# Performance work log

Hardware: AMD Instinct MI355X
Metric: run time of the kernel (lower is better)

The kernel has to match this reference:

```python
import jax, jax.numpy as jnp
import numpy as np

B, K, D, LS, NL = 32, 64, 256, 128, 2


def _xavier(key, shape):
    # torch xavier_uniform for Linear weight [out, in]
    fan_out, fan_in = shape[-2], shape[-1]
    lim = float(np.sqrt(6.0 / (fan_in + fan_out)))
    return jax.random.uniform(key, shape, jnp.float32, -lim, lim)


def setup_inputs():
    key = jax.random.key(0)
    ks = jax.random.split(key, 32)
    inp = {
        "X": jax.random.normal(ks[0], (B, K, D), jnp.float32),
        # per-layer stacked params [NL, ...]
        "k_w": _xavier(ks[1], (NL, D, D)),
        "q_w": _xavier(ks[2], (NL, D, D)),
        "rv_w1": _xavier(ks[3], (NL, D, 2 * D)),
        "rv_b1": jnp.zeros((NL, D), jnp.float32),
        "rv_w2": _xavier(ks[4], (NL, D, D)),
        "rv_b2": jnp.zeros((NL, D), jnp.float32),
        "ln_g": jnp.ones((NL, D), jnp.float32),
        "ln_b": jnp.zeros((NL, D), jnp.float32),
        "mlp_w1": _xavier(ks[5], (NL, D, D)),
        "mlp_b1": jnp.zeros((NL, D), jnp.float32),
        "mlp_w2": _xavier(ks[6], (NL, D, D)),
        "mlp_b2": jnp.zeros((NL, D), jnp.float32),
        "proj_w": _xavier(ks[7], (LS, D)),
        "proj_b": jnp.zeros((LS,), jnp.float32),
        "mu_w": _xavier(ks[8], (LS, LS)),
        "mu_b": jnp.zeros((LS,), jnp.float32),
        "sp_w": _xavier(ks[9], (LS, LS)),
        "sp_b": jnp.zeros((LS,), jnp.float32),
    }
    return inp


def _gelu(x):
    return jax.nn.gelu(x, approximate=False)


def _layernorm(x, g, b, eps=1e-5):
    m = jnp.mean(x, axis=-1, keepdims=True)
    v = jnp.mean((x - m) ** 2, axis=-1, keepdims=True)
    return (x - m) / jnp.sqrt(v + eps) * g + b


def _block(x, kw, qw, rw1, rb1, rw2, rb2, lg, lb, mw1, mb1, mw2, mb2):
    scale = D ** (-0.5)
    x_orig = x
    # pairwise difference r[b,i,j,:] = x[b,i]-x[b,j]
    r = x[:, :, None, :] - x[:, None, :, :]                      # [B,K,K,D]
    xi = jnp.broadcast_to(x[:, :, None, :], (B, K, K, D))
    cat = jnp.concatenate([xi, r], axis=-1)                      # [B,K,K,2D]
    v = _gelu(jnp.einsum('bijc,dc->bijd', cat, rw1) + rb1)
    v = jnp.einsum('bijd,ed->bije', v, rw2) + rb2                # [B,K,K,D]
    k = jnp.einsum('bid,ed->bie', x, kw)
    q = jnp.einsum('bid,ed->bie', x, qw) * scale
    attn = jax.nn.softmax(jnp.einsum('bid,bjd->bij', q, k), axis=2)
    agg = jnp.einsum('bij,bijd->bid', attn, v)
    h = _layernorm(x_orig + agg, lg, lb)
    h = jnp.einsum('bid,ed->bie', _gelu(jnp.einsum('bid,ed->bie', h, mw1) + mb1), mw2) + mb2
    return x_orig + h


def reference(X, k_w, q_w, rv_w1, rv_b1, rv_w2, rv_b2, ln_g, ln_b,
              mlp_w1, mlp_b1, mlp_w2, mlp_b2, proj_w, proj_b,
              mu_w, mu_b, sp_w, sp_b):
    x = X
    for i in range(NL):
        x = _block(x, k_w[i], q_w[i], rv_w1[i], rv_b1[i], rv_w2[i], rv_b2[i],
                   ln_g[i], ln_b[i], mlp_w1[i], mlp_b1[i], mlp_w2[i], mlp_b2[i])
    s = jnp.sum(x, axis=1)                                        # [B,D]
    h = _gelu(s @ proj_w.T + proj_b)                              # [B,LS]
    mu = h @ mu_w.T + mu_b
    scale = jax.nn.softplus(h @ sp_w.T + sp_b)
    return (mu, scale)
```

## Files before the change

### kernel.cpp

```cpp
#include <hip/hip_runtime.h>
#include <hip/hip_bf16.h>


using bf16 = __hip_bfloat16;
typedef short bf16x8 __attribute__((ext_vector_type(8)));
typedef float f32x4 __attribute__((ext_vector_type(4)));

__device__ __forceinline__ float bfu(unsigned short u) { return __uint_as_float(((unsigned)u) << 16); }

__device__ __forceinline__ unsigned short bfr(float v) {
  unsigned u = __float_as_uint(v);
  u += 0x7FFFu + ((u >> 16) & 1u);
  return (unsigned short)(u >> 16);
}

__device__ __forceinline__ float gelu_e(float x) {
  return 0.5f * x * (1.0f + erff(x * 0.7071067811865475f));
}

__device__ __forceinline__ float load_f(const void* p, int i, int fl) {
  if (fl) return bfu(((const unsigned short*)p)[i]);
  return ((const float*)p)[i];
}

__device__ __forceinline__ int block_detect(const void* X) {
  __shared__ int bad_s;
  if (threadIdx.x == 0) bad_s = 0;
  __syncthreads();
  if (threadIdx.x < 256) {
    const float v = bfu(((const unsigned short*)X)[threadIdx.x]);
    if (!(fabsf(v) < 1e6f)) atomicOr(&bad_s, 1);
  }
  __syncthreads();
  return bad_s ? 0 : 1;
}

__device__ __forceinline__ void stage_split4(unsigned short (&aF)[2][4096], int row, int d0, float4 v) {
  ushort4 h, lo;
  h.x = bfr(v.x); h.y = bfr(v.y); h.z = bfr(v.z); h.w = bfr(v.w);
  lo.x = bfr(v.x - bfu(h.x)); lo.y = bfr(v.y - bfu(h.y));
  lo.z = bfr(v.z - bfu(h.z)); lo.w = bfr(v.w - bfu(h.w));
  const int kt = d0 >> 5, lane = row | (((d0 >> 3) & 3) << 4), j = d0 & 7;
  *(ushort4*)&aF[0][kt*512 + lane*8 + j] = h;
  *(ushort4*)&aF[1][kt*512 + lane*8 + j] = lo;
}

__device__ void prep_phase(
    int blk, int t, int fl, char* psm,
    const void* kw, const void* qw, const void* rw1, const void* rw2,
    const void* mw1, const void* mw2, const void* pw, const void* muw, const void* spw,
    const void* rb1, const void* rb2, const void* lng, const void* lnb,
    const void* mb1, const void* mb2, const void* pb, const void* mub, const void* spb,
    unsigned short* wfb, unsigned short* w3b, float* wh, float* bc)
{
  if (blk < 16) {
    unsigned short* ls = (unsigned short*)psm;
    unsigned* lsu = (unsigned*)psm;
    const int l = blk >> 3, kt = blk & 7;
    #pragma unroll
    for (int pass = 0; pass < 2; ++pass) {
      if (pass == 0) {
        if (fl) {
          #pragma unroll
          for (int s = 0; s < 2; ++s) {
            const unsigned* sp = (const unsigned*)((s == 0) ? kw : qw);
            for (int i = t; i < 4096; i += 512) {
              const int e = i >> 4, d2 = i & 15;
              lsu[s*4096 + i] = sp[(l*256 + e)*128 + kt*16 + d2];
            }
          }
        } else {
          #pragma unroll
          for (int s = 0; s < 2; ++s) {
            const float* sp = (const float*)((s == 0) ? kw : qw);
            for (int i = t; i < 4096; i += 512) {
              const int e = i >> 4, d2 = i & 15;
              const float f0 = sp[(l*256 + e)*256 + kt*32 + d2*2];
              const float f1 = sp[(l*256 + e)*256 + kt*32 + d2*2 + 1];
              lsu[s*4096 + i] = (unsigned)bfr(f0) | ((unsigned)bfr(f1) << 16);
            }
          }
        }
      } else {
        if (fl) {
          const unsigned* sp = (const unsigned*)rw1;
          #pragma unroll
          for (int s = 0; s < 2; ++s)
            for (int i = t; i < 4096; i += 512) {
              const int e = i >> 4, d2 = i & 15;
              lsu[s*4096 + i] = sp[(l*256 + e)*256 + s*128 + kt*16 + d2];
            }
        } else {
          const float* sp = (const float*)rw1;
          #pragma unroll
          for (int s = 0; s < 2; ++s)
            for (int i = t; i < 4096; i += 512) {
              const int e = i >> 4, d2 = i & 15;
              const float f0 = sp[(l*256 + e)*512 + s*256 + kt*32 + d2*2];
              const float f1 = sp[(l*256 + e)*512 + s*256 + kt*32 + d2*2 + 1];
              lsu[s*4096 + i] = (unsigned)bfr(f0) | ((unsigned)bfr(f1) << 16);
            }
        }
      }
      __syncthreads();
      unsigned* outp = (unsigned*)wfb + (l*8 + kt)*16384 + pass*8192;
      for (int f2 = t; f2 < 8192; f2 += 512) {
        const int j2 = f2 & 3, lane = (f2 >> 2) & 63, ntl = f2 >> 8;
        const int seg = ntl >> 4;
        const int e = (ntl & 15)*16 + (lane & 15);
        const int dl = ((lane >> 4) & 3)*8 + j2*2;
        unsigned short r0 = ls[seg*8192 + e*32 + dl];
        unsigned short r1 = ls[seg*8192 + e*32 + dl + 1];
        if (pass == 1 && seg == 0) {
          const unsigned short w0 = ls[8192 + e*32 + dl];
          const unsigned short w1 = ls[8192 + e*32 + dl + 1];
          r0 = bfr(bfu(r0) + bfu(w0)); r1 = bfr(bfu(r1) + bfu(w1));
        }
        outp[f2] = (unsigned)r0 | ((unsigned)r1 << 16);
      }
      __syncthreads();
    }
    return;
  }
  int b2 = blk - 16;
  if (b2 < 48) {
    unsigned short* ls = (unsigned short*)psm;
    unsigned* lsu = (unsigned*)psm;
    const int l3 = b2 >> 3, kt = b2 & 7;
    const int l = l3 / 3, gm = l3 % 3;
    const void* src = (gm == 0) ? rw2 : (gm == 1) ? mw1 : mw2;
    if (fl) {
      const unsigned* sp = (const unsigned*)src;
      for (int i = t; i < 4096; i += 512) {
        const int e = i >> 4, d2 = i & 15;
        lsu[i] = sp[(l*256 + e)*128 + kt*16 + d2];
      }
    } else {
      const float* sp = (const float*)src;
      for (int i = t; i < 4096; i += 512) {
        const int e = i >> 4, d2 = i & 15;
        const float f0 = sp[(l*256 + e)*256 + kt*32 + d2*2];
        const float f1 = sp[(l*256 + e)*256 + kt*32 + d2*2 + 1];
        lsu[i] = (unsigned)bfr(f0) | ((unsigned)bfr(f1) << 16);
      }
    }
    __syncthreads();
    unsigned* outp = (unsigned*)w3b + (l3*8 + kt)*4096;
    for (int f2 = t; f2 < 4096; f2 += 512) {
      const int j2 = f2 & 3, lane = (f2 >> 2) & 63, nt = f2 >> 8;
      const int e = nt*16 + (lane & 15);
      const int dl = ((lane >> 4) & 3)*8 + j2*2;
      outp[f2] = (unsigned)ls[e*32 + dl] | ((unsigned)ls[e*32 + dl + 1] << 16);
    }
    return;
  }
  b2 -= 48;
  if (b2 < 24) {
    float* lsf = (float*)psm;
    if (b2 < 8) {
      const int l0 = b2*16;
      if (fl) {
        const unsigned* sp = (const unsigned*)pw;
        for (int i = t; i < 2048; i += 512) {
          const int ll = i >> 7, d2 = i & 127;
          const unsigned u = sp[(l0 + ll)*128 + d2];
          lsf[ll*256 + d2*2]     = __uint_as_float(u << 16);
          lsf[ll*256 + d2*2 + 1] = __uint_as_float(u & 0xffff0000u);
        }
      } else {
        const float* sp = (const float*)pw;
        for (int i = t; i < 4096; i += 512) {
          const int ll = i >> 8, d = i & 255;
          lsf[ll*256 + d] = sp[(l0 + ll)*256 + d];
        }
      }
      __syncthreads();
      for (int i = t; i < 4096; i += 512) {
        const int d = i >> 4, ll = i & 15;
        wh[d*128 + l0 + ll] = lsf[ll*256 + d];
      }
    } else {
      const int grp2 = b2 - 8;
      const int isSp = grp2 >> 3;
      const int l0 = (grp2 & 7)*16;
      const void* src = isSp ? spw : muw;
      const int off = isSp ? 49152 : 32768;
      if (fl) {
        const unsigned* sp = (const unsigned*)src;
        for (int i = t; i < 1024; i += 512) {
          const int ll = i >> 6, c2 = i & 63;
          const unsigned u = sp[(l0 + ll)*64 + c2];
          lsf[ll*128 + c2*2]     = __uint_as_float(u << 16);
          lsf[ll*128 + c2*2 + 1] = __uint_as_float(u & 0xffff0000u);
        }
      } else {
        const float* sp = (const float*)src;
        for (int i = t; i < 2048; i += 512) {
          const int ll = i >> 7, c = i & 127;
          lsf[ll*128 + c] = sp[(l0 + ll)*128 + c];
        }
      }
      __syncthreads();
      for (int i = t; i < 2048; i += 512) {
        const int c = i >> 4, ll = i & 15;
        wh[off + c*128 + l0 + ll] = lsf[ll*128 + c];
      }
    }
    return;
  }
  if (b2 == 24) {
    for (int i = t; i < 3456; i += 512) {
      const void* src; int off;
      if (i < 512)       { src = rb1; off = i; }
      else if (i < 1024) { src = rb2; off = i - 512; }
      else if (i < 1536) { src = lng; off = i - 1024; }
      else if (i < 2048) { src = lnb; off = i - 1536; }
      else if (i < 2560) { src = mb1; off = i - 2048; }
      else if (i < 3072) { src = mb2; off = i - 2560; }
      else if (i < 3200) { src = pb;  off = i - 3072; }
      else if (i < 3328) { src = mub; off = i - 3200; }
      else               { src = spb; off = i - 3328; }
      bc[i] = load_f(src, off, fl);
    }
  }
}

__device__ __forceinline__ bf16x8 raw_bfrag(int seg, int e, int d0, int fl,
    const void* kw, const void* qw, const void* rw1)
{
  if (fl) {
    if (seg == 0) return *(const bf16x8*)((const unsigned short*)kw + e*256 + d0);
    if (seg == 1) return *(const bf16x8*)((const unsigned short*)qw + e*256 + d0);
    const unsigned short* r1 = (const unsigned short*)rw1 + e*512;
    const bf16x8 wb = *(const bf16x8*)(r1 + 256 + d0);
    if (seg == 3) return wb;
    const bf16x8 wa = *(const bf16x8*)(r1 + d0);
    bf16x8 r;
    #pragma unroll
    for (int i = 0; i < 8; ++i)
      r[i] = (short)bfr(bfu((unsigned short)wa[i]) + bfu((unsigned short)wb[i]));
    return r;
  } else {
    float vs[8];
    if (seg <= 1) {
      const float* sp = (const float*)((seg == 0) ? kw : qw) + e*256 + d0;
      #pragma unroll
      for (int i = 0; i < 8; ++i) vs[i] = sp[i];
    } else {
      const float* r1 = (const float*)rw1 + e*512;
      #pragma unroll
      for (int i = 0; i < 8; ++i) vs[i] = r1[256 + d0 + i];
      if (seg == 2) {
        #pragma unroll
        for (int i = 0; i < 8; ++i) vs[i] += r1[d0 + i];
      }
    }
    bf16x8 r;
    #pragma unroll
    for (int i = 0; i < 8; ++i) r[i] = (short)bfr(vs[i]);
    return r;
  }
}

template<bool SPLIT>
__device__ void k1_raw(const unsigned short (&aF)[2][4096], int seg, int ntg0,
    const void* kw, const void* qw, const void* rw1, const void* rb1, int fl,
    float* __restrict__ kq, float* __restrict__ Pf, unsigned* __restrict__ Qpk,
    int row0, int t)
{
  const int w = t >> 6, l64 = t & 63;
  const int col = l64 & 15, quad = l64 >> 4;
  f32x4 acc[2];
  acc[0] = (f32x4){0.f, 0.f, 0.f, 0.f};
  acc[1] = (f32x4){0.f, 0.f, 0.f, 0.f};
  for (int kt = 0; kt < 8; ++kt) {
    const bf16x8 ah = *(const bf16x8*)&aF[0][kt*512 + l64*8];
    bf16x8 al;
    if (SPLIT) al = *(const bf16x8*)&aF[1][kt*512 + l64*8];
    const int d0 = kt*32 + quad*8;
    #pragma unroll
    for (int i = 0; i < 2; ++i) {
      const int ntg = ntg0 + w*2 + i;
      const int e = (ntg & 15)*16 + col;
      const bf16x8 b = raw_bfrag(seg, e, d0, fl, kw, qw, rw1);
      acc[i] = __builtin_amdgcn_mfma_f32_16x16x32_bf16(ah, b, acc[i], 0, 0, 0);
      if (SPLIT) acc[i] = __builtin_amdgcn_mfma_f32_16x16x32_bf16(al, b, acc[i], 0, 0, 0);
    }
  }
  #pragma unroll
  for (int i = 0; i < 2; ++i) {
    const int ntg = ntg0 + w*2 + i;
    if (seg < 2) {
      const int n = ntg*16 + col;
      #pragma unroll
      for (int r = 0; r < 4; ++r)
        kq[(size_t)(row0 + quad*4 + r)*512 + n] = acc[i][r];
    } else if (seg == 2) {
      const int c = (ntg & 15)*16 + col;
      const float bias = load_f(rb1, c, fl);
      #pragma unroll
      for (int r = 0; r < 4; ++r)
        Pf[(size_t)(row0 + quad*4 + r)*256 + c] = acc[i][r] + bias;
    } else {
      #pragma unroll
      for (int r = 0; r < 4; ++r) {
        const float v = acc[i][r];
        const float pv = __shfl_xor(v, 1, 64);
        if (!(col & 1)) {
          const unsigned uu = (unsigned)bfr(v) | ((unsigned)bfr(pv) << 16);
          Qpk[(size_t)(row0 + quad*4 + r)*128 + (ntg & 15)*8 + (col >> 1)] = uu;
        }
      }
    }
  }
}

__global__ __launch_bounds__(512) void fusedA(
    const void* __restrict__ X, const void* __restrict__ kw, const void* __restrict__ qw,
    const void* __restrict__ rw1, const void* __restrict__ rw2, const void* __restrict__ mw1,
    const void* __restrict__ mw2, const void* __restrict__ pw, const void* __restrict__ muw,
    const void* __restrict__ spw,
    const void* __restrict__ rb1, const void* __restrict__ rb2, const void* __restrict__ lng,
    const void* __restrict__ lnb, const void* __restrict__ mb1, const void* __restrict__ mb2,
    const void* __restrict__ pb, const void* __restrict__ mub, const void* __restrict__ spb,
    unsigned short* __restrict__ wfb, unsigned short* __restrict__ w3b,
    float* __restrict__ wh, float* __restrict__ bc,
    float* __restrict__ kq, float* __restrict__ Pf, unsigned* __restrict__ Qpk)
{
  __shared__ __align__(16) char smem[32768];
  const int fl = block_detect(X);
  const int t = threadIdx.x;
  const int blk = blockIdx.x;
  if (blk < 89) {
    prep_phase(blk, t, fl, smem, kw, qw, rw1, rw2, mw1, mw2, pw, muw, spw,
               rb1, rb2, lng, lnb, mb1, mb2, pb, mub, spb, wfb, w3b, wh, bc);
    return;
  }
  auto& aF = *(unsigned short(*)[2][4096])smem;
  const int rb = blk - 89;
  const int mb = rb >> 2, seg = rb & 3;
  const int row0 = mb * 16, ntg0 = seg * 16;
  if (fl) {
    const int row = t >> 5, d0 = (t & 31) * 8;
    const uint4 u = *(const uint4*)((const unsigned*)X + (size_t)(row0 + row)*128 + (t & 31)*4);
    const int kt = d0 >> 5, lane = row | (((d0 >> 3) & 3) << 4);
    *(uint4*)&aF[0][kt*512 + lane*8] = u;
  } else {
    for (int i = t; i < 1024; i += 512) {
      const int row = i >> 6, d0 = (i & 63) * 4;
      stage_split4(aF, row, d0, *(const float4*)((const float*)X + (size_t)(row0 + row)*256 + d0));
    }
  }
  __syncthreads();
  if (fl) k1_raw<false>(aF, seg, ntg0, kw, qw, rw1, rb1, fl, kq, Pf, Qpk, row0, t);
  else    k1_raw<true >(aF, seg, ntg0, kw, qw, rw1, rb1, fl, kq, Pf, Qpk, row0, t);
}

template<bool SPLIT, int NTG>
__device__ __forceinline__ void k1_body(
    const unsigned short (&aF)[2][4096],
    const unsigned short* __restrict__ wfb, const float* __restrict__ bc,
    float* __restrict__ kq, float* __restrict__ Pf, unsigned* __restrict__ Qpk,
    int l, int row0, int ntg0, int t)
{
  const int w = t >> 6, l64 = t & 63;
  const int col = l64 & 15, quad = l64 >> 4;
  f32x4 acc[NTG];
  #pragma unroll
  for (int i = 0; i < NTG; ++i) acc[i] = (f32x4){0.f, 0.f, 0.f, 0.f};
  for (int kt = 0; kt < 8; ++kt) {
    const bf16x8 ah = *(const bf16x8*)&aF[0][kt*512 + l64*8];
    bf16x8 al;
    if (SPLIT) al = *(const bf16x8*)&aF[1][kt*512 + l64*8];
    #pragma unroll
    for (int i = 0; i < NTG; ++i) {
      const int ntg = ntg0 + w*NTG + i;
      const bf16x8 b = *(const bf16x8*)&wfb[((l*8 + kt)*64 + ntg)*512 + l64*8];
      acc[i] = __builtin_amdgcn_mfma_f32_16x16x32_bf16(ah, b, acc[i], 0, 0, 0);
      if (SPLIT) acc[i] = __builtin_amdgcn_mfma_f32_16x16x32_bf16(al, b, acc[i], 0, 0, 0);
    }
  }
  #pragma unroll
  for (int i = 0; i < NTG; ++i) {
    const int ntg = ntg0 + w*NTG + i;
    if (ntg < 32) {
      const int n = ntg*16 + col;
      #pragma unroll
      for (int r = 0; r < 4; ++r)
        kq[(size_t)(row0 + quad*4 + r)*512 + n] = acc[i][r];
    } else if (ntg < 48) {
      const int c = (ntg - 32)*16 + col;
      const float bias = bc[l*256 + c];
      #pragma unroll
      for (int r = 0; r < 4; ++r)
        Pf[(size_t)(row0 + quad*4 + r)*256 + c] = acc[i][r] + bias;
    } else {
      #pragma unroll
      for (int r = 0; r < 4; ++r) {
        const float v = acc[i][r];
        const float pv = __shfl_xor(v, 1, 64);
        if (!(col & 1)) {
          const unsigned uu = (unsigned)bfr(v) | ((unsigned)bfr(pv) << 16);
          Qpk[(size_t)(row0 + quad*4 + r)*128 + (ntg - 48)*8 + (col >> 1)] = uu;
        }
      }
    }
  }
}

__global__ __launch_bounds__(256) void k23_attn(
    const float* __restrict__ kq, const float* __restrict__ Pf,
    const unsigned* __restrict__ Qpk, float* __restrict__ g,
    float* __restrict__ ssacc, unsigned* __restrict__ cnt, int doZero)
{
  __shared__ float qs[2][256];
  __shared__ float scp[2][64];
  __shared__ float als[2][64];
  const int t = threadIdx.x;
  const int b = (int)blockIdx.x >> 5, ip = (int)blockIdx.x & 31;
  const int base = b << 6, i0 = ip * 2;
  if (doZero && ip == 0) {
    ssacc[b*256 + t] = 0.f;
    if (t == 0) cnt[b] = 0u;
  }
  for (int i = t; i < 512; i += 256)
    qs[i >> 8][i & 255] = kq[(size_t)(base + i0 + (i >> 8))*512 + 256 + (i & 255)];
  __syncthreads();
  {
    const int w = t >> 6, lane = t & 63;
    const int jl = lane & 15, part = lane >> 4;
    const int j = w*16 + jl;
    const float* krow = kq + (size_t)(base + j)*512 + part*64;
    const float* q0p = &qs[0][part*64];
    const float* q1p = &qs[1][part*64];
    float s0 = 0.f, s1 = 0.f;
    for (int dd = 0; dd < 64; dd += 4) {
      const float4 kv = *(const float4*)&krow[dd];
      const float4 q0 = *(const float4*)&q0p[dd];
      const float4 q1 = *(const float4*)&q1p[dd];
      s0 = fmaf(kv.x, q0.x, s0); s0 = fmaf(kv.y, q0.y, s0);
      s0 = fmaf(kv.z, q0.z, s0); s0 = fmaf(kv.w, q0.w, s0);
      s1 = fmaf(kv.x, q1.x, s1); s1 = fmaf(kv.y, q1.y, s1);
      s1 = fmaf(kv.z, q1.z, s1); s1 = fmaf(kv.w, q1.w, s1);
    }
    s0 += __shfl_xor(s0, 16, 64); s0 += __shfl_xor(s0, 32, 64);
    s1 += __shfl_xor(s1, 16, 64); s1 += __shfl_xor(s1, 32, 64);
    if (part == 0) { scp[0][j] = s0 * 0.0625f; scp[1][j] = s1 * 0.0625f; }
  }
  __syncthreads();
  if (t < 128) {
    const int row = t >> 6, j = t & 63;
    float s = scp[row][j];
    float m = s;
    #pragma unroll
    for (int off = 32; off; off >>= 1) m = fmaxf(m, __shfl_xor(m, off, 64));
    const float e = __expf(s - m);
    float ss = e;
    #pragma unroll
    for (int off = 32; off; off >>= 1) ss += __shfl_xor(ss, off, 64);
    als[row][j] = e / ss;
  }
  __syncthreads();
  const int rg = t >> 7, cp = t & 127;
  const int r = base + i0 + rg;
  const float2 P = *(const float2*)&Pf[(size_t)r*256 + cp*2];
  const float A0 = -1.702f * P.x, A1 = -1.702f * P.y;
  const float* ap = &als[rg][0];
  const unsigned* qp = Qpk + (size_t)base*128 + cp;
  float acc0 = 0.f, acc1 = 0.f;
  #pragma unroll 8
  for (int j = 0; j < 64; ++j) {
    const unsigned u = qp[j*128];
    const float wgt = ap[j];
    const float q0 = __uint_as_float(u << 16);
    const float q1 = __uint_as_float(u & 0xffff0000u);
    const float s0 = __builtin_amdgcn_rcpf(1.f + __expf(fmaf(1.702f, q0, A0)));
    const float s1 = __builtin_amdgcn_rcpf(1.f + __expf(fmaf(1.702f, q1, A1)));
    acc0 = fmaf(wgt * (P.x - q0), s0, acc0);
    acc1 = fmaf(wgt * (P.y - q1), s1, acc1);
  }
  *(float2*)&g[(size_t)r*256 + cp*2] = make_float2(acc0, acc1);
}

__device__ __forceinline__ void k4_gemm8(
    f32x4 acc[2], const unsigned short (&aF)[2][4096],
    const unsigned short* __restrict__ wg, int w, int l64)
{
  acc[0] = (f32x4){0.f, 0.f, 0.f, 0.f};
  acc[1] = (f32x4){0.f, 0.f, 0.f, 0.f};
  for (int kt = 0; kt < 8; ++kt) {
    const bf16x8 ah = *(const bf16x8*)&aF[0][kt*512 + l64*8];
    const bf16x8 al = *(const bf16x8*)&aF[1][kt*512 + l64*8];
    #pragma unroll
    for (int nt = 0; nt < 2; ++nt) {
      const bf16x8 b = *(const bf16x8*)&wg[((kt*16 + (w*2 + nt))*64 + l64)*8];
      acc[nt] = __builtin_amdgcn_mfma_f32_16x16x32_bf16(ah, b, acc[nt], 0, 0, 0);
      acc[nt] = __builtin_amdgcn_mfma_f32_16x16x32_bf16(al, b, acc[nt], 0, 0, 0);
    }
  }
}

template<bool ADAPT, bool TAIL, int NR>
__device__ __forceinline__ void k4_core(
    const float* __restrict__ g, const void* __restrict__ xin, int fl,
    float* __restrict__ xout, const unsigned short* __restrict__ wg,
    const float* __restrict__ bc, int l, int row0, int t, bool writeX,
    unsigned short (&aF)[2][4096], float* bufB, float (&mv)[16][2])
{
  const int w = t >> 6, l64 = t & 63;
  const int col = l64 & 15, quad = l64 >> 4;
  const float* rb2c = bc + 512  + l*256;
  const float* lngc = bc + 1024 + l*256;
  const float* lnbc = bc + 1536 + l*256;
  const float* mb1c = bc + 2048 + l*256;
  const float* mb2c = bc + 2560 + l*256;

  for (int i = t; i < NR*64; i += 512) {
    const int row = i >> 6, d0 = (i & 63) * 4;
    stage_split4(aF, row, d0, *(const float4*)&g[(size_t)(row0 + row)*256 + d0]);
  }
  if (ADAPT && fl) {
    for (int c = t; c < NR*128; c += 512) {
      const int row = c >> 7, dp = c & 127;
      const unsigned u = ((const unsigned*)xin)[(size_t)(row0 + row)*128 + dp];
      bufB[row*260 + dp*2]     = __uint_as_float(u << 16);
      bufB[row*260 + dp*2 + 1] = __uint_as_float(u & 0xffff0000u);
    }
  } else {
    for (int c = t; c < NR*64; c += 512) {
      const int row = c >> 6, d0 = (c & 63) * 4;
      *(float4*)&bufB[row*260 + d0] = *(const float4*)((const float*)xin + (size_t)(row0 + row)*256 + d0);
    }
  }
  __syncthreads();
  float xtr[2][4];
  #pragma unroll
  for (int nt = 0; nt < 2; ++nt) {
    const int cn = (w*2 + nt)*16 + col;
    #pragma unroll
    for (int r = 0; r < 4; ++r) xtr[nt][r] = bufB[(quad*4 + r)*260 + cn];
  }
  __syncthreads();

  f32x4 acc[2];
  k4_gemm8(acc, aF, wg, w, l64);
  #pragma unroll
  for (int nt = 0; nt < 2; ++nt) {
    const int cn = (w*2 + nt)*16 + col;
    #pragma unroll
    for (int r = 0; r < 4; ++r)
      bufB[(quad*4 + r)*260 + cn] = acc[nt][r] + rb2c[cn] + xtr[nt][r];
  }
  __syncthreads();
  {
    const int row = t >> 5, part = t & 31;
    if (row < NR) {
      float s = 0.f, s2 = 0.f;
      #pragma unroll
      for (int kk = 0; kk < 8; ++kk) {
        const float v = bufB[row*260 + part + kk*32];
        s += v; s2 = fmaf(v, v, s2);
      }
      #pragma unroll
      for (int off = 16; off; off >>= 1) {
        s  += __shfl_xor(s, off, 32);
        s2 += __shfl_xor(s2, off, 32);
      }
      if (part == 0) {
        const float mu = s * (1.f/256.f);
        mv[row][0] = mu;
        mv[row][1] = rsqrtf(fmaf(-mu, mu, s2 * (1.f/256.f)) + 1e-5f);
      }
    }
  }
  __syncthreads();
  for (int i = t; i < NR*64; i += 512) {
    const int row = i >> 6, d0 = (i & 63) * 4;
    float4 v = *(const float4*)&bufB[row*260 + d0];
    const float m = mv[row][0], iv = mv[row][1];
    v.x = (v.x - m)*iv*lngc[d0]   + lnbc[d0];
    v.y = (v.y - m)*iv*lngc[d0+1] + lnbc[d0+1];
    v.z = (v.z - m)*iv*lngc[d0+2] + lnbc[d0+2];
    v.w = (v.w - m)*iv*lngc[d0+3] + lnbc[d0+3];
    stage_split4(aF, row, d0, v);
  }
  __syncthreads();
  k4_gemm8(acc, aF, wg + 65536, w, l64);
  #pragma unroll
  for (int nt = 0; nt < 2; ++nt) {
    const int cn = (w*2 + nt)*16 + col;
    #pragma unroll
    for (int r = 0; r < 4; ++r)
      if (quad*4 + r < NR)
        bufB[(quad*4 + r)*260 + cn] = gelu_e(acc[nt][r] + mb1c[cn]);
  }
  __syncthreads();
  for (int i = t; i < NR*64; i += 512) {
    const int row = i >> 6, d0 = (i & 63) * 4;
    stage_split4(aF, row, d0, *(const float4*)&bufB[row*260 + d0]);
  }
  __syncthreads();
  k4_gemm8(acc, aF, wg + 2*65536, w, l64);
  if (TAIL) {
    #pragma unroll
    for (int nt = 0; nt < 2; ++nt) {
      const int cn = (w*2 + nt)*16 + col;
      #pragma unroll
      for (int r = 0; r < 4; ++r)
        bufB[(quad*4 + r)*260 + cn] = acc[nt][r] + mb2c[cn] + xtr[nt][r];
    }
    __syncthreads();
    for (int i = t; i < NR*64; i += 512) {
      const int row = i >> 6, d0 = (i & 63) * 4;
      const float4 v = *(const float4*)&bufB[row*260 + d0];
      if (writeX) *(float4*)&xout[(size_t)(row0 + row)*256 + d0] = v;
      stage_split4(aF, row, d0, v);
    }
    __syncthreads();
  } else {
    #pragma unroll
    for (int nt = 0; nt < 2; ++nt) {
      const int cn = (w*2 + nt)*16 + col;
      #pragma unroll
      for (int r = 0; r < 4; ++r)
        if (quad*4 + r < NR)
          xout[(size_t)(row0 + quad*4 + r)*256 + cn] = acc[nt][r] + mb2c[cn] + xtr[nt][r];
    }
  }
}

__global__ __launch_bounds__(512) void k41_mix_kq(
    const float* __restrict__ g, const unsigned short* __restrict__ w3b,
    const unsigned short* __restrict__ wfb, const float* __restrict__ bc,
    const void* __restrict__ X, float* __restrict__ x,
    float* __restrict__ kq, float* __restrict__ Pf, unsigned* __restrict__ Qpk)
{
  const int fl = block_detect(X);
  __shared__ __align__(16) unsigned short aF[2][4096];
  __shared__ float bufB[16*260];
  __shared__ float mv[16][2];
  const int t = threadIdx.x;
  const int rb = (int)blockIdx.x >> 1, parity = (int)blockIdx.x & 1;
  const int row0 = rb * 16;
  k4_core<true, true, 16>(g, X, fl, x, w3b, bc, 0, row0, t, parity == 0, aF, bufB, mv);
  k1_body<true, 4>(aF, wfb, bc, kq, Pf, Qpk, 1, row0, parity*32, t);
}

__global__ __launch_bounds__(512) void k4_fin_head(
    const float* __restrict__ g, const unsigned short* __restrict__ w3b,
    const float* __restrict__ bc, float* __restrict__ x,
    const float* __restrict__ wh, float* __restrict__ ssacc,
    unsigned* __restrict__ cnt, const void* __restrict__ X,
    void* __restrict__ out)
{
  const int fl = block_detect(X);
  __shared__ __align__(16) unsigned short aF[2][4096];
  __shared__ float bufB[16*260];
  __shared__ float mv[16][2];
  __shared__ int lastf;
  const int t = threadIdx.x;
  const int row0 = (int)blockIdx.x * 8;
  const int b = (int)blockIdx.x >> 3;
  k4_core<false, true, 8>(g, x, 0, x, w3b + 3*65536, bc, 1, row0, t, false, aF, bufB, mv);
  if (t < 256) {
    float cs = 0.f;
    #pragma unroll
    for (int r = 0; r < 8; ++r) cs += bufB[r*260 + t];
    atomicAdd(&ssacc[b*256 + t], cs);
  }
  __syncthreads();
  if (t == 0) lastf = (atomicAdd(&cnt[b], 1u) == 7u);
  __syncthreads();
  if (!lastf) return;
  float* ss = bufB;
  float* hh = bufB + 256;
  if (t < 256)
    ss[t] = __hip_atomic_load(&ssacc[b*256 + t], __ATOMIC_RELAXED, __HIP_MEMORY_SCOPE_AGENT);
  __syncthreads();
  if (t < 128) {
    float acc = bc[3072 + t];
    const float* projT = wh;
    for (int d = 0; d < 256; ++d) acc = fmaf(ss[d], projT[d*128 + t], acc);
    hh[t] = gelu_e(acc);
  }
  __syncthreads();
  if (t < 256) {
    float v; int oidx;
    if (t < 128) {
      float acc = bc[3200 + t];
      const float* muT = wh + 32768;
      for (int c = 0; c < 128; ++c) acc = fmaf(hh[c], muT[c*128 + t], acc);
      v = acc; oidx = b*128 + t;
    } else {
      const int u = t - 128;
      float acc = bc[3328 + u];
      const float* spT = wh + 49152;
      for (int c = 0; c < 128; ++c) acc = fmaf(hh[c], spT[c*128 + u], acc);
      v = (acc > 20.f) ? acc : log1pf(__expf(acc));
      oidx = 4096 + b*128 + u;
    }
    if (fl) ((bf16*)out)[oidx] = __float2bfloat16(v);
    else    ((float*)out)[oidx] = v;
  }
}

extern "C" void kernel_launch(void* const* d_in, const int* in_sizes, int n_in,
                              void* d_out, int out_size, void* d_ws, size_t ws_size,
                              hipStream_t stream)
{
  (void)in_sizes; (void)n_in; (void)out_size; (void)ws_size;
  float* ws    = (float*)d_ws;
  float* x     = ws + 16;
  float* kq    = x + 524288;
  float* Pf    = kq + 1048576;
  unsigned* Qpk = (unsigned*)(Pf + 524288);
  float* g     = (float*)(Qpk + 262144);
  unsigned short* wfb = (unsigned short*)(g + 524288);
  unsigned short* w3b = wfb + 524288;
  float* wh    = (float*)(w3b + 393216);
  float* bc    = wh + 65536;
  float* ssacc = bc + 4096;
  unsigned* cnt = (unsigned*)(ssacc + 8192);

  fusedA<<<dim3(601), dim3(512), 0, stream>>>(
      d_in[0], d_in[1], d_in[2], d_in[3], d_in[5], d_in[9], d_in[11],
      d_in[13], d_in[15], d_in[17],
      d_in[4], d_in[6], d_in[7], d_in[8], d_in[10], d_in[12],
      d_in[14], d_in[16], d_in[18],
      wfb, w3b, wh, bc, kq, Pf, Qpk);
  k23_attn<<<dim3(1024), dim3(256), 0, stream>>>(kq, Pf, Qpk, g, ssacc, cnt, 0);
  k41_mix_kq<<<dim3(256), dim3(512), 0, stream>>>(g, w3b, wfb, bc, d_in[0], x, kq, Pf, Qpk);
  k23_attn<<<dim3(1024), dim3(256), 0, stream>>>(kq, Pf, Qpk, g, ssacc, cnt, 1);
  k4_fin_head<<<dim3(256), dim3(512), 0, stream>>>(g, w3b, bc, x, wh, ssacc, cnt, d_in[0], (void*)d_out);
}
```

Before: 212.2 us.

## Fuse attention with the following MLP stage via last-arriver counters, cutting launches

Merges the attention kernel with the per-row-tile mix/MLP kernel. Each group of four attention blocks covering a 16-row tile increments a counter, and the last block to arrive runs the LayerNorm/MLP and next-layer projections for that tile. kq/Pf/Qpk are double-buffered so the fused kernel can write the next layer's inputs without racing readers. Counter and accumulator zeroing moves into the prep phase, and layer-0 weight repacking blocks are dropped. This removes two launches and their inter-kernel gaps. In exchange it serializes the tail work onto fewer blocks and relies on threadfence/atomic ordering.

```diff
diff --git a/kernel.cpp b/kernel.cpp
--- a/kernel.cpp
+++ b/kernel.cpp
@@ -51,12 +51,13 @@
     const void* mw1, const void* mw2, const void* pw, const void* muw, const void* spw,
     const void* rb1, const void* rb2, const void* lng, const void* lnb,
     const void* mb1, const void* mb2, const void* pb, const void* mub, const void* spb,
-    unsigned short* wfb, unsigned short* w3b, float* wh, float* bc)
-{
-  if (blk < 16) {
+    unsigned short* wfb, unsigned short* w3b, float* wh, float* bc,
+    unsigned* cnts, float* ssacc)
+{
+  if (blk < 8) {
     unsigned short* ls = (unsigned short*)psm;
     unsigned* lsu = (unsigned*)psm;
-    const int l = blk >> 3, kt = blk & 7;
+    const int l = 1, kt = blk;
     #pragma unroll
     for (int pass = 0; pass < 2; ++pass) {
       if (pass == 0) {
@@ -103,7 +104,7 @@
         }
       }
       __syncthreads();
-      unsigned* outp = (unsigned*)wfb + (l*8 + kt)*16384 + pass*8192;
+      unsigned* outp = (unsigned*)wfb + (8 + kt)*16384 + pass*8192;
       for (int f2 = t; f2 < 8192; f2 += 512) {
         const int j2 = f2 & 3, lane = (f2 >> 2) & 63, ntl = f2 >> 8;
         const int seg = ntl >> 4;
@@ -122,7 +123,7 @@
     }
     return;
   }
-  int b2 = blk - 16;
+  int b2 = blk - 8;
   if (b2 < 48) {
     unsigned short* ls = (unsigned short*)psm;
     unsigned* lsu = (unsigned*)psm;
@@ -222,6 +223,8 @@
       else               { src = spb; off = i - 3328; }
       bc[i] = load_f(src, off, fl);
     }
+    for (int i = t; i < 288; i += 512) cnts[i] = 0u;
+    for (int i = t; i < 8192; i += 512) ssacc[i] = 0.f;
   }
 }
 
@@ -325,19 +328,21 @@
     const void* __restrict__ pb, const void* __restrict__ mub, const void* __restrict__ spb,
     unsigned short* __restrict__ wfb, unsigned short* __restrict__ w3b,
     float* __restrict__ wh, float* __restrict__ bc,
-    float* __restrict__ kq, float* __restrict__ Pf, unsigned* __restrict__ Qpk)
+    unsigned* __restrict__ cnts, float* __restrict__ ssacc,
+    float* __restrict__ kqA, float* __restrict__ PfA, unsigned* __restrict__ QpkA)
 {
   __shared__ __align__(16) char smem[32768];
   const int fl = block_detect(X);
   const int t = threadIdx.x;
   const int blk = blockIdx.x;
-  if (blk < 89) {
+  if (blk < 81) {
     prep_phase(blk, t, fl, smem, kw, qw, rw1, rw2, mw1, mw2, pw, muw, spw,
-               rb1, rb2, lng, lnb, mb1, mb2, pb, mub, spb, wfb, w3b, wh, bc);
+               rb1, rb2, lng, lnb, mb1, mb2, pb, mub, spb, wfb, w3b, wh, bc,
+               cnts, ssacc);
     return;
   }
   auto& aF = *(unsigned short(*)[2][4096])smem;
-  const int rb = blk - 89;
+  const int rb = blk - 81;
   const int mb = rb >> 2, seg = rb & 3;
   const int row0 = mb * 16, ntg0 = seg * 16;
   if (fl) {
@@ -352,8 +357,8 @@
     }
   }
   __syncthreads();
-  if (fl) k1_raw<false>(aF, seg, ntg0, kw, qw, rw1, rb1, fl, kq, Pf, Qpk, row0, t);
-  else    k1_raw<true >(aF, seg, ntg0, kw, qw, rw1, rb1, fl, kq, Pf, Qpk, row0, t);
+  if (fl) k1_raw<false>(aF, seg, ntg0, kw, qw, rw1, rb1, fl, kqA, PfA, QpkA, row0, t);
+  else    k1_raw<true >(aF, seg, ntg0, kw, qw, rw1, rb1, fl, kqA, PfA, QpkA, row0, t);
 }
 
 template<bool SPLIT, int NTG>
@@ -408,80 +413,6 @@
   }
 }
 
-__global__ __launch_bounds__(256) void k23_attn(
-    const float* __restrict__ kq, const float* __restrict__ Pf,
-    const unsigned* __restrict__ Qpk, float* __restrict__ g,
-    float* __restrict__ ssacc, unsigned* __restrict__ cnt, int doZero)
-{
-  __shared__ float qs[2][256];
-  __shared__ float scp[2][64];
-  __shared__ float als[2][64];
-  const int t = threadIdx.x;
-  const int b = (int)blockIdx.x >> 5, ip = (int)blockIdx.x & 31;
-  const int base = b << 6, i0 = ip * 2;
-  if (doZero && ip == 0) {
-    ssacc[b*256 + t] = 0.f;
-    if (t == 0) cnt[b] = 0u;
-  }
-  for (int i = t; i < 512; i += 256)
-    qs[i >> 8][i & 255] = kq[(size_t)(base + i0 + (i >> 8))*512 + 256 + (i & 255)];
-  __syncthreads();
-  {
-    const int w = t >> 6, lane = t & 63;
-    const int jl = lane & 15, part = lane >> 4;
-    const int j = w*16 + jl;
-    const float* krow = kq + (size_t)(base + j)*512 + part*64;
-    const float* q0p = &qs[0][part*64];
-    const float* q1p = &qs[1][part*64];
-    float s0 = 0.f, s1 = 0.f;
-    for (int dd = 0; dd < 64; dd += 4) {
-      const float4 kv = *(const float4*)&krow[dd];
-      const float4 q0 = *(const float4*)&q0p[dd];
-      const float4 q1 = *(const float4*)&q1p[dd];
-      s0 = fmaf(kv.x, q0.x, s0); s0 = fmaf(kv.y, q0.y, s0);
-      s0 = fmaf(kv.z, q0.z, s0); s0 = fmaf(kv.w, q0.w, s0);
-      s1 = fmaf(kv.x, q1.x, s1); s1 = fmaf(kv.y, q1.y, s1);
-      s1 = fmaf(kv.z, q1.z, s1); s1 = fmaf(kv.w, q1.w, s1);
-    }
-    s0 += __shfl_xor(s0, 16, 64); s0 += __shfl_xor(s0, 32, 64);
-    s1 += __shfl_xor(s1, 16, 64); s1 += __shfl_xor(s1, 32, 64);
-    if (part == 0) { scp[0][j] = s0 * 0.0625f; scp[1][j] = s1 * 0.0625f; }
-  }
-  __syncthreads();
-  if (t < 128) {
-    const int row = t >> 6, j = t & 63;
-    float s = scp[row][j];
-    float m = s;
-    #pragma unroll
-    for (int off = 32; off; off >>= 1) m = fmaxf(m, __shfl_xor(m, off, 64));
-    const float e = __expf(s - m);
-    float ss = e;
-    #pragma unroll
-    for (int off = 32; off; off >>= 1) ss += __shfl_xor(ss, off, 64);
-    als[row][j] = e / ss;
-  }
-  __syncthreads();
-  const int rg = t >> 7, cp = t & 127;
-  const int r = base + i0 + rg;
-  const float2 P = *(const float2*)&Pf[(size_t)r*256 + cp*2];
-  const float A0 = -1.702f * P.x, A1 = -1.702f * P.y;
-  const float* ap = &als[rg][0];
-  const unsigned* qp = Qpk + (size_t)base*128 + cp;
-  float acc0 = 0.f, acc1 = 0.f;
-  #pragma unroll 8
-  for (int j = 0; j < 64; ++j) {
-    const unsigned u = qp[j*128];
-    const float wgt = ap[j];
-    const float q0 = __uint_as_float(u << 16);
-    const float q1 = __uint_as_float(u & 0xffff0000u);
-    const float s0 = __builtin_amdgcn_rcpf(1.f + __expf(fmaf(1.702f, q0, A0)));
-    const float s1 = __builtin_amdgcn_rcpf(1.f + __expf(fmaf(1.702f, q1, A1)));
-    acc0 = fmaf(wgt * (P.x - q0), s0, acc0);
-    acc1 = fmaf(wgt * (P.y - q1), s1, acc1);
-  }
-  *(float2*)&g[(size_t)r*256 + cp*2] = make_float2(acc0, acc1);
-}
-
 __device__ __forceinline__ void k4_gemm8(
     f32x4 acc[2], const unsigned short (&aF)[2][4096],
     const unsigned short* __restrict__ wg, int w, int l64)
@@ -500,7 +431,7 @@
   }
 }
 
-template<bool ADAPT, bool TAIL, int NR>
+template<bool ADAPT>
 __device__ __forceinline__ void k4_core(
     const float* __restrict__ g, const void* __restrict__ xin, int fl,
     float* __restrict__ xout, const unsigned short* __restrict__ wg,
@@ -515,19 +446,19 @@
   const float* mb1c = bc + 2048 + l*256;
   const float* mb2c = bc + 2560 + l*256;
 
-  for (int i = t; i < NR*64; i += 512) {
+  for (int i = t; i < 1024; i += 512) {
     const int row = i >> 6, d0 = (i & 63) * 4;
     stage_split4(aF, row, d0, *(const float4*)&g[(size_t)(row0 + row)*256 + d0]);
   }
   if (ADAPT && fl) {
-    for (int c = t; c < NR*128; c += 512) {
+    for (int c = t; c < 2048; c += 512) {
       const int row = c >> 7, dp = c & 127;
       const unsigned u = ((const unsigned*)xin)[(size_t)(row0 + row)*128 + dp];
       bufB[row*260 + dp*2]     = __uint_as_float(u << 16);
       bufB[row*260 + dp*2 + 1] = __uint_as_float(u & 0xffff0000u);
     }
   } else {
-    for (int c = t; c < NR*64; c += 512) {
+    for (int c = t; c < 1024; c += 512) {
       const int row = c >> 6, d0 = (c & 63) * 4;
       *(float4*)&bufB[row*260 + d0] = *(const float4*)((const float*)xin + (size_t)(row0 + row)*256 + d0);
     }
@@ -554,27 +485,25 @@
   __syncthreads();
   {
     const int row = t >> 5, part = t & 31;
-    if (row < NR) {
-      float s = 0.f, s2 = 0.f;
-      #pragma unroll
-      for (int kk = 0; kk < 8; ++kk) {
-        const float v = bufB[row*260 + part + kk*32];
-        s += v; s2 = fmaf(v, v, s2);
-      }
-      #pragma unroll
-      for (int off = 16; off; off >>= 1) {
-        s  += __shfl_xor(s, off, 32);
-        s2 += __shfl_xor(s2, off, 32);
-      }
-      if (part == 0) {
-        const float mu = s * (1.f/256.f);
-        mv[row][0] = mu;
-        mv[row][1] = rsqrtf(fmaf(-mu, mu, s2 * (1.f/256.f)) + 1e-5f);
-      }
-    }
-  }
-  __syncthreads();
-  for (int i = t; i < NR*64; i += 512) {
+    float s = 0.f, s2 = 0.f;
+    #pragma unroll
+    for (int kk = 0; kk < 8; ++kk) {
+      const float v = bufB[row*260 + part + kk*32];
+      s += v; s2 = fmaf(v, v, s2);
+    }
+    #pragma unroll
+    for (int off = 16; off; off >>= 1) {
+      s  += __shfl_xor(s, off, 32);
+      s2 += __shfl_xor(s2, off, 32);
+    }
+    if (part == 0) {
+      const float mu = s * (1.f/256.f);
+      mv[row][0] = mu;
+      mv[row][1] = rsqrtf(fmaf(-mu, mu, s2 * (1.f/256.f)) + 1e-5f);
+    }
+  }
+  __syncthreads();
+  for (int i = t; i < 1024; i += 512) {
     const int row = i >> 6, d0 = (i & 63) * 4;
     float4 v = *(const float4*)&bufB[row*260 + d0];
     const float m = mv[row][0], iv = mv[row][1];
@@ -591,87 +520,138 @@
     const int cn = (w*2 + nt)*16 + col;
     #pragma unroll
     for (int r = 0; r < 4; ++r)
-      if (quad*4 + r < NR)
-        bufB[(quad*4 + r)*260 + cn] = gelu_e(acc[nt][r] + mb1c[cn]);
-  }
-  __syncthreads();
-  for (int i = t; i < NR*64; i += 512) {
+      bufB[(quad*4 + r)*260 + cn] = gelu_e(acc[nt][r] + mb1c[cn]);
+  }
+  __syncthreads();
+  for (int i = t; i < 1024; i += 512) {
     const int row = i >> 6, d0 = (i & 63) * 4;
     stage_split4(aF, row, d0, *(const float4*)&bufB[row*260 + d0]);
   }
   __syncthreads();
   k4_gemm8(acc, aF, wg + 2*65536, w, l64);
-  if (TAIL) {
-    #pragma unroll
-    for (int nt = 0; nt < 2; ++nt) {
-      const int cn = (w*2 + nt)*16 + col;
-      #pragma unroll
-      for (int r = 0; r < 4; ++r)
-        bufB[(quad*4 + r)*260 + cn] = acc[nt][r] + mb2c[cn] + xtr[nt][r];
-    }
-    __syncthreads();
-    for (int i = t; i < NR*64; i += 512) {
-      const int row = i >> 6, d0 = (i & 63) * 4;
-      const float4 v = *(const float4*)&bufB[row*260 + d0];
-      if (writeX) *(float4*)&xout[(size_t)(row0 + row)*256 + d0] = v;
-      stage_split4(aF, row, d0, v);
-    }
-    __syncthreads();
-  } else {
-    #pragma unroll
-    for (int nt = 0; nt < 2; ++nt) {
-      const int cn = (w*2 + nt)*16 + col;
-      #pragma unroll
-      for (int r = 0; r < 4; ++r)
-        if (quad*4 + r < NR)
-          xout[(size_t)(row0 + quad*4 + r)*256 + cn] = acc[nt][r] + mb2c[cn] + xtr[nt][r];
-    }
-  }
-}
-
-__global__ __launch_bounds__(512) void k41_mix_kq(
-    const float* __restrict__ g, const unsigned short* __restrict__ w3b,
-    const unsigned short* __restrict__ wfb, const float* __restrict__ bc,
+  #pragma unroll
+  for (int nt = 0; nt < 2; ++nt) {
+    const int cn = (w*2 + nt)*16 + col;
+    #pragma unroll
+    for (int r = 0; r < 4; ++r)
+      bufB[(quad*4 + r)*260 + cn] = acc[nt][r] + mb2c[cn] + xtr[nt][r];
+  }
+  __syncthreads();
+  for (int i = t; i < 1024; i += 512) {
+    const int row = i >> 6, d0 = (i & 63) * 4;
+    const float4 v = *(const float4*)&bufB[row*260 + d0];
+    if (writeX) *(float4*)&xout[(size_t)(row0 + row)*256 + d0] = v;
+    stage_split4(aF, row, d0, v);
+  }
+  __syncthreads();
+}
+
+__global__ __launch_bounds__(512) void k23m(
+    const float* __restrict__ kq, const float* __restrict__ Pf,
+    const unsigned* __restrict__ Qpk, float* __restrict__ g,
     const void* __restrict__ X, float* __restrict__ x,
-    float* __restrict__ kq, float* __restrict__ Pf, unsigned* __restrict__ Qpk)
-{
+    const unsigned short* __restrict__ w3b, const unsigned short* __restrict__ wfb,
+    const float* __restrict__ bc, const float* __restrict__ wh,
+    float* __restrict__ kqO, float* __restrict__ PfO, unsigned* __restrict__ QpkO,
+    float* __restrict__ ssacc, unsigned* __restrict__ cnts,
+    void* __restrict__ out, int mode)
+{
+  __shared__ __align__(16) char smem[33280];
+  __shared__ float mv[16][2];
+  __shared__ int winf;
   const int fl = block_detect(X);
-  __shared__ __align__(16) unsigned short aF[2][4096];
-  __shared__ float bufB[16*260];
-  __shared__ float mv[16][2];
   const int t = threadIdx.x;
-  const int rb = (int)blockIdx.x >> 1, parity = (int)blockIdx.x & 1;
-  const int row0 = rb * 16;
-  k4_core<true, true, 16>(g, X, fl, x, w3b, bc, 0, row0, t, parity == 0, aF, bufB, mv);
-  k1_body<true, 4>(aF, wfb, bc, kq, Pf, Qpk, 1, row0, parity*32, t);
-}
-
-__global__ __launch_bounds__(512) void k4_fin_head(
-    const float* __restrict__ g, const unsigned short* __restrict__ w3b,
-    const float* __restrict__ bc, float* __restrict__ x,
-    const float* __restrict__ wh, float* __restrict__ ssacc,
-    unsigned* __restrict__ cnt, const void* __restrict__ X,
-    void* __restrict__ out)
-{
-  const int fl = block_detect(X);
-  __shared__ __align__(16) unsigned short aF[2][4096];
-  __shared__ float bufB[16*260];
-  __shared__ float mv[16][2];
-  __shared__ int lastf;
-  const int t = threadIdx.x;
-  const int row0 = (int)blockIdx.x * 8;
-  const int b = (int)blockIdx.x >> 3;
-  k4_core<false, true, 8>(g, x, 0, x, w3b + 3*65536, bc, 1, row0, t, false, aF, bufB, mv);
+  const int b = (int)blockIdx.x >> 4, qd = (int)blockIdx.x & 15;
+  const int base = b << 6, i0 = qd * 4;
+  float* qs  = (float*)smem;
+  float* scp = qs + 1024;
+  float* als = scp + 256;
+
+  for (int i = t; i < 1024; i += 512)
+    qs[i] = kq[(size_t)(base + i0 + (i >> 8))*512 + 256 + (i & 255)];
+  __syncthreads();
+  {
+    const int w = t >> 6, lane = t & 63;
+    const int r = w & 3, jh = w >> 2;
+    const int jl = lane & 31, dh = lane >> 5;
+    const int j = jh*32 + jl;
+    const float* krow = kq + (size_t)(base + j)*512 + dh*128;
+    const float* qp = qs + r*256 + dh*128;
+    float s = 0.f;
+    for (int dd = 0; dd < 128; dd += 4) {
+      const float4 kv = *(const float4*)&krow[dd];
+      const float4 qv = *(const float4*)&qp[dd];
+      s = fmaf(kv.x, qv.x, s); s = fmaf(kv.y, qv.y, s);
+      s = fmaf(kv.z, qv.z, s); s = fmaf(kv.w, qv.w, s);
+    }
+    s += __shfl_xor(s, 32, 64);
+    if (dh == 0) scp[r*64 + j] = s * 0.0625f;
+  }
+  __syncthreads();
+  if (t < 256) {
+    const int row = t >> 6, j = t & 63;
+    float s = scp[row*64 + j];
+    float m = s;
+    #pragma unroll
+    for (int off = 32; off; off >>= 1) m = fmaxf(m, __shfl_xor(m, off, 64));
+    const float e = __expf(s - m);
+    float ss = e;
+    #pragma unroll
+    for (int off = 32; off; off >>= 1) ss += __shfl_xor(ss, off, 64);
+    als[row*64 + j] = e / ss;
+  }
+  __syncthreads();
+  {
+    const int rg = t >> 7, cp = t & 127;
+    const int r = base + i0 + rg;
+    const float2 P = *(const float2*)&Pf[(size_t)r*256 + cp*2];
+    const float A0 = -1.702f * P.x, A1 = -1.702f * P.y;
+    const float* ap = als + rg*64;
+    const unsigned* qp = Qpk + (size_t)base*128 + cp;
+    float acc0 = 0.f, acc1 = 0.f;
+    #pragma unroll 8
+    for (int j = 0; j < 64; ++j) {
+      const unsigned u = qp[j*128];
+      const float wgt = ap[j];
+      const float q0 = __uint_as_float(u << 16);
+      const float q1 = __uint_as_float(u & 0xffff0000u);
+      const float s0 = __builtin_amdgcn_rcpf(1.f + __expf(fmaf(1.702f, q0, A0)));
+      const float s1 = __builtin_amdgcn_rcpf(1.f + __expf(fmaf(1.702f, q1, A1)));
+      acc0 = fmaf(wgt * (P.x - q0), s0, acc0);
+      acc1 = fmaf(wgt * (P.y - q1), s1, acc1);
+    }
+    *(float2*)&g[(size_t)r*256 + cp*2] = make_float2(acc0, acc1);
+  }
+  const int rt = (int)blockIdx.x >> 2;
+  __syncthreads();
+  if (t == 0) {
+    __threadfence();
+    winf = (atomicAdd(&cnts[(mode ? 128 : 0) + rt], 1u) == 3u);
+  }
+  __syncthreads();
+  if (!winf) return;
+  __threadfence();
+  __syncthreads();
+
+  auto& aF = *(unsigned short(*)[2][4096])smem;
+  float* bufB = (float*)(smem + 16384);
+  const int row0 = rt * 16;
+  if (mode == 0) {
+    k4_core<true>(g, X, fl, x, w3b, bc, 0, row0, t, true, aF, bufB, mv);
+    k1_body<true, 8>(aF, wfb, bc, kqO, PfO, QpkO, 1, row0, 0, t);
+    return;
+  }
+  k4_core<false>(g, x, 0, x, w3b + 3*65536, bc, 1, row0, t, false, aF, bufB, mv);
   if (t < 256) {
     float cs = 0.f;
     #pragma unroll
-    for (int r = 0; r < 8; ++r) cs += bufB[r*260 + t];
+    for (int r = 0; r < 16; ++r) cs += bufB[r*260 + t];
     atomicAdd(&ssacc[b*256 + t], cs);
   }
   __syncthreads();
-  if (t == 0) lastf = (atomicAdd(&cnt[b], 1u) == 7u);
-  __syncthreads();
-  if (!lastf) return;
+  if (t == 0) winf = (atomicAdd(&cnts[256 + b], 1u) == 3u);
+  __syncthreads();
+  if (!winf) return;
   float* ss = bufB;
   float* hh = bufB + 256;
   if (t < 256)
@@ -711,25 +691,30 @@
   (void)in_sizes; (void)n_in; (void)out_size; (void)ws_size;
   float* ws    = (float*)d_ws;
   float* x     = ws + 16;
-  float* kq    = x + 524288;
-  float* Pf    = kq + 1048576;
-  unsigned* Qpk = (unsigned*)(Pf + 524288);
-  float* g     = (float*)(Qpk + 262144);
+  float* kqA   = x + 524288;
+  float* PfA   = kqA + 1048576;
+  unsigned* QpkA = (unsigned*)(PfA + 524288);
+  float* kqB   = (float*)(QpkA + 262144);
+  float* PfB   = kqB + 1048576;
+  unsigned* QpkB = (unsigned*)(PfB + 524288);
+  float* g     = (float*)(QpkB + 262144);
   unsigned short* wfb = (unsigned short*)(g + 524288);
   unsigned short* w3b = wfb + 524288;
   float* wh    = (float*)(w3b + 393216);
   float* bc    = wh + 65536;
   float* ssacc = bc + 4096;
-  unsigned* cnt = (unsigned*)(ssacc + 8192);
-
-  fusedA<<<dim3(601), dim3(512), 0, stream>>>(
+  unsigned* cnts = (unsigned*)(ssacc + 8192);
+
+  fusedA<<<dim3(593), dim3(512), 0, stream>>>(
       d_in[0], d_in[1], d_in[2], d_in[3], d_in[5], d_in[9], d_in[11],
       d_in[13], d_in[15], d_in[17],
       d_in[4], d_in[6], d_in[7], d_in[8], d_in[10], d_in[12],
       d_in[14], d_in[16], d_in[18],
-      wfb, w3b, wh, bc, kq, Pf, Qpk);
-  k23_attn<<<dim3(1024), dim3(256), 0, stream>>>(kq, Pf, Qpk, g, ssacc, cnt, 0);
-  k41_mix_kq<<<dim3(256), dim3(512), 0, stream>>>(g, w3b, wfb, bc, d_in[0], x, kq, Pf, Qpk);
-  k23_attn<<<dim3(1024), dim3(256), 0, stream>>>(kq, Pf, Qpk, g, ssacc, cnt, 1);
-  k4_fin_head<<<dim3(256), dim3(512), 0, stream>>>(g, w3b, bc, x, wh, ssacc, cnt, d_in[0], (void*)d_out);
-}
+      wfb, w3b, wh, bc, cnts, ssacc, kqA, PfA, QpkA);
+  k23m<<<dim3(512), dim3(512), 0, stream>>>(
+      kqA, PfA, QpkA, g, d_in[0], x, w3b, wfb, bc, wh,
+      kqB, PfB, QpkB, ssacc, cnts, (void*)d_out, 0);
+  k23m<<<dim3(512), dim3(512), 0, stream>>>(
+      kqB, PfB, QpkB, g, d_in[0], x, w3b, wfb, bc, wh,
+      kqB, PfB, QpkB, ssacc, cnts, (void*)d_out, 1);
+}
```

After: 329.3 us. 55.2% more time.
